# Optimization experiments

Measured on AMD Instinct MI355X. Metric: run time of the kernel, lower is better.

## Reference

```python
import jax, jax.numpy as jnp
import numpy as np

VOCAB = 32000
DIM = 1024
DFF = 4096
NLLM = 3
B, S = 2, 2048
THRESH = 0.98
EPS = 1e-8


def setup_inputs() -> dict:
    key = jax.random.key(0)
    ks = jax.random.split(key, 5)
    x = jax.random.randint(ks[0], (B, S), 0, VOCAB)
    emb = 0.02 * jax.random.normal(ks[1], (VOCAB, DIM), jnp.float32)
    ln_g = jnp.ones((NLLM, DIM), jnp.float32)
    ln_b = jnp.zeros((NLLM, DIM), jnp.float32)
    W1 = 0.002 * jax.random.normal(ks[2], (NLLM, DIM, DFF), jnp.float32)
    b1 = jnp.zeros((NLLM, DFF), jnp.float32)
    W2 = 0.002 * jax.random.normal(ks[3], (NLLM, DFF, DIM), jnp.float32)
    b2 = jnp.zeros((NLLM, DIM), jnp.float32)
    W_out = (1.0 / np.sqrt(DIM)) * jax.random.normal(ks[4], (VOCAB, DIM), jnp.float32)
    return dict(x=x, emb=emb, ln_g=ln_g, ln_b=ln_b, W1=W1, b1=b1, W2=W2, b2=b2, W_out=W_out)


def _layernorm(h, g, b):
    m = jnp.mean(h, axis=-1, keepdims=True)
    v = jnp.var(h, axis=-1, keepdims=True)
    return (h - m) * jax.lax.rsqrt(v + 1e-5) * g + b


def reference(x, emb, ln_g, ln_b, W1, b1, W2, b2, W_out):
    # Cascaded early-exit ensemble. The torch code physically re-packs surviving
    # tokens; since each LLM block here is per-token (residual MLP), a masked
    # formulation computes identical per-token math and is jit-compatible.
    Bb, Ss = x.shape
    T = Bb * Ss
    h = emb[x.reshape(T)]                      # [T, D] token embeddings
    active = jnp.ones((T,), dtype=bool)
    final = jnp.zeros((T, VOCAB), dtype=h.dtype)
    for i in range(NLLM):                      # fixed, small number of LLMs
        hn = _layernorm(h, ln_g[i], ln_b[i])
        mlp = jax.nn.gelu(hn @ W1[i] + b1[i]) @ W2[i] + b2[i]
        h_out = h + mlp                        # [T, D]
        logits = h_out @ W_out.T               # [T, V] shared output head
        cos = jnp.sum(h * h_out, axis=-1) / (
            jnp.linalg.norm(h, axis=-1) * jnp.linalg.norm(h_out, axis=-1) + EPS)
        is_last = (i == NLLM - 1)
        should_exit = cos >= THRESH
        take = active if is_last else (active & should_exit)
        final = jnp.where(take[:, None], logits, final)   # scatter logits for exiting tokens
        active = active & (~take)
        h = jnp.where(active[:, None], h_out, h)          # continuing tokens carry h_out forward
    return final.reshape(Bb, Ss, VOCAB)
```

## Files before the change

kernel.cpp:

```cpp
#include <hip/hip_runtime.h>
#include <hip/hip_bf16.h>
#include <stdint.h>

constexpr int TK   = 4096;
constexpr int DIMC = 1024;
constexpr int DFFC = 4096;
constexpr int VOC  = 32000;
constexpr int NL   = 3;

typedef __attribute__((ext_vector_type(8))) short bf16x8;
typedef __attribute__((ext_vector_type(8))) _Float16 half8;
typedef __attribute__((ext_vector_type(4))) float f32x4;
using u16 = unsigned short;

__device__ __forceinline__ u16 f2bf(float f) {
  unsigned int u = __float_as_uint(f);
  u += 0x7FFF + ((u >> 16) & 1);
  return (u16)(u >> 16);
}

__device__ __forceinline__ void split16(float v, u16& hi, u16& lo) {
  _Float16 a = (_Float16)v;
  _Float16 b = (_Float16)(v - (float)a);
  hi = __builtin_bit_cast(u16, a);
  lo = __builtin_bit_cast(u16, b);
}

__device__ __forceinline__ float gelu_f(float x) {
  float x3 = x * x * x;
  return 0.5f * x * (1.0f + tanhf(0.7978845608028654f * (x + 0.044715f * x3)));
}

__device__ __forceinline__ void gll16(const void* g, void* l) {
  __builtin_amdgcn_global_load_lds(
      (const __attribute__((address_space(1))) unsigned int*)g,
      (__attribute__((address_space(3))) unsigned int*)l, 16, 0, 0);
}

__global__ __launch_bounds__(256) void k_init(const int* __restrict__ x,
    const float* __restrict__ emb, float* __restrict__ h,
    int* __restrict__ surv, int* __restrict__ cnts) {
  const int t = blockIdx.x, tid = threadIdx.x;
  if (t == 0 && tid < 16) cnts[tid] = (tid == 12) ? TK : 0;
  if (tid == 0) surv[t] = t;
  const int tok = x[t];
  ((float4*)(h + (size_t)t * DIMC))[tid] =
      ((const float4*)(emb + (size_t)tok * DIMC))[tid];
}

__global__ __launch_bounds__(256) void k_ln(const float* __restrict__ h,
    const int* __restrict__ surv, const int* __restrict__ pM,
    const float* __restrict__ g, const float* __restrict__ b,
    u16* __restrict__ hn1, u16* __restrict__ hn2) {
  const int bidx = blockIdx.x;
  if (bidx >= *pM) return;
  const int t = surv[bidx];
  const int tid = threadIdx.x;
  const int lane = tid & 63, wid = tid >> 6;
  __shared__ float sm[4];
  float4 v = ((const float4*)(h + (size_t)t * DIMC))[tid];
  float s = v.x + v.y + v.z + v.w;
#pragma unroll
  for (int o = 32; o; o >>= 1) s += __shfl_down(s, o);
  if (lane == 0) sm[wid] = s;
  __syncthreads();
  const float mean = (sm[0] + sm[1] + sm[2] + sm[3]) * (1.0f / DIMC);
  __syncthreads();
  float4 d;
  d.x = v.x - mean; d.y = v.y - mean; d.z = v.z - mean; d.w = v.w - mean;
  float q = d.x * d.x + d.y * d.y + d.z * d.z + d.w * d.w;
#pragma unroll
  for (int o = 32; o; o >>= 1) q += __shfl_down(q, o);
  if (lane == 0) sm[wid] = q;
  __syncthreads();
  const float var = (sm[0] + sm[1] + sm[2] + sm[3]) * (1.0f / DIMC);
  const float rstd = 1.0f / sqrtf(var + 1e-5f);
  float4 gg = ((const float4*)g)[tid];
  float4 bb = ((const float4*)b)[tid];
  float o4[4];
  o4[0] = (d.x * rstd * gg.x + bb.x) * 16.f;
  o4[1] = (d.y * rstd * gg.y + bb.y) * 16.f;
  o4[2] = (d.z * rstd * gg.z + bb.z) * 16.f;
  o4[3] = (d.w * rstd * gg.w + bb.w) * 16.f;
  ushort4 u1, u2;
  split16(o4[0], u1.x, u2.x); split16(o4[1], u1.y, u2.y);
  split16(o4[2], u1.z, u2.z); split16(o4[3], u1.w, u2.w);
  ((ushort4*)(hn1 + (size_t)bidx * DIMC))[tid] = u1;
  ((ushort4*)(hn2 + (size_t)bidx * DIMC))[tid] = u2;
}

__global__ __launch_bounds__(256) void k_splitw_all(
    const float* __restrict__ W1, const float* __restrict__ W2,
    u16* __restrict__ W1all, u16* __restrict__ W2all)
{
  int bid = blockIdx.x;
  const int s = bid >> 11; bid &= 2047;
  const int tens = bid >> 10; bid &= 1023;
  const float* W; int K, N; u16 *O1, *O2; int bk, bn;
  if (tens == 0) {
    W = W1 + (size_t)s * DIMC * DFFC; K = DIMC; N = DFFC;
    O1 = W1all + (size_t)s * 2 * DFFC * DIMC;
    O2 = O1 + (size_t)DFFC * DIMC;
    bk = (bid & 15) * 64; bn = (bid >> 4) * 64;
  } else {
    W = W2 + (size_t)s * DFFC * DIMC; K = DFFC; N = DIMC;
    O1 = W2all + (size_t)s * 2 * DIMC * DFFC;
    O2 = O1 + (size_t)DIMC * DFFC;
    bk = (bid >> 4) * 64; bn = (bid & 15) * 64;
  }
  __shared__ float t[64][65];
  const int lx = threadIdx.x & 63, ly = threadIdx.x >> 6;
#pragma unroll
  for (int i = 0; i < 64; i += 4)
    t[ly + i][lx] = W[(size_t)(bk + ly + i) * N + bn + lx];
  __syncthreads();
  const int n4 = threadIdx.x >> 4;
  const int kq = (threadIdx.x & 15) * 4;
#pragma unroll
  for (int j = 0; j < 4; ++j) {
    const int n = j * 16 + n4;
    ushort4 h1, h2;
    {
      float v0 = t[kq + 0][n] * 256.f, v1 = t[kq + 1][n] * 256.f;
      float v2 = t[kq + 2][n] * 256.f, v3 = t[kq + 3][n] * 256.f;
      split16(v0, h1.x, h2.x); split16(v1, h1.y, h2.y);
      split16(v2, h1.z, h2.z); split16(v3, h1.w, h2.w);
    }
    const size_t o = (size_t)(bn + n) * K + bk + kq;
    *(ushort4*)&O1[o] = h1;
    *(ushort4*)&O2[o] = h2;
  }
}

__global__ __launch_bounds__(256) void k_cvtb(const float* __restrict__ in,
    u16* __restrict__ o, int n4) {
  int i = blockIdx.x * blockDim.x + threadIdx.x;
  const int stride = gridDim.x * blockDim.x;
  for (; i < n4; i += stride) {
    float4 v = ((const float4*)in)[i];
    ushort4 u;
    u.x = f2bf(v.x); u.y = f2bf(v.y); u.z = f2bf(v.z); u.w = f2bf(v.w);
    ((ushort4*)o)[i] = u;
  }
}

__global__ __launch_bounds__(512, 1) void k_mlp1(
    const u16* __restrict__ wsb,
    int offA, int pstrA,
    int offB, int pstrB,
    const int* __restrict__ pM,
    const float* __restrict__ bias,
    u16* __restrict__ O1, u16* __restrict__ O2)
{
  const int x = blockIdx.x & 7, g = blockIdx.x >> 3;
  const int rb = g & 15;
  const int cb = x * 2 + (g >> 4);
  const int M = *pM;
  if (rb * 256 >= M) return;
  const int n0 = cb * 256;

  __shared__ u16 S[2][32768];
  const int tid = threadIdx.x, w = tid >> 6, l = tid & 63;
  const int lr16 = l & 15, hi = l >> 4;

  int goff[8];
#pragma unroll
  for (int q = 0; q < 8; ++q) {
    const int bi = w * 8 + q;
    const int side = bi >> 5;
    const int pl = (bi >> 4) & 1;
    const int j = bi & 15;
    const int row = (side ? n0 : rb * 256) + j * 16 + lr16;
    const int base = side ? (offB + pl * pstrB) : (offA + pl * pstrA);
    goff[q] = base + row * DIMC + hi * 8;
  }

  const int wr = w >> 2, wc = w & 3;
  f32x4 acc[8][4];
#pragma unroll
  for (int mi = 0; mi < 8; ++mi)
#pragma unroll
    for (int ni = 0; ni < 4; ++ni) acc[mi][ni] = (f32x4){0.f, 0.f, 0.f, 0.f};

  auto STAGE = [&](int buf, int kt) {
#pragma unroll
    for (int q = 0; q < 8; ++q)
      gll16(wsb + (size_t)(goff[q] + kt * 32), (void*)&S[buf][(w * 8 + q) * 512]);
  };

  STAGE(0, 0);
  STAGE(1, 1);
  const int NT = DIMC / 32;
  for (int kt = 0; kt < NT; ++kt) {
    const int cur = kt & 1;
    if (kt + 1 < NT) asm volatile("s_waitcnt vmcnt(8)" ::: "memory");
    else             asm volatile("s_waitcnt vmcnt(0)" ::: "memory");
    __builtin_amdgcn_s_barrier();
    half8 b1v[4], b2v[4];
#pragma unroll
    for (int ni = 0; ni < 4; ++ni) {
      const int sub = (32 + wc * 4 + ni) * 512 + l * 8;
      b1v[ni] = *(const half8*)&S[cur][sub];
      b2v[ni] = *(const half8*)&S[cur][sub + 8192];
    }
#pragma unroll
    for (int mh = 0; mh < 2; ++mh) {
      half8 a1v[4], a2v[4];
#pragma unroll
      for (int i = 0; i < 4; ++i) {
        const int sub = (wr * 8 + mh * 4 + i) * 512 + l * 8;
        a1v[i] = *(const half8*)&S[cur][sub];
        a2v[i] = *(const half8*)&S[cur][sub + 8192];
      }
      __builtin_amdgcn_s_setprio(1);
#pragma unroll
      for (int i = 0; i < 4; ++i)
#pragma unroll
        for (int ni = 0; ni < 4; ++ni) {
          f32x4 c = acc[mh * 4 + i][ni];
          c = __builtin_amdgcn_mfma_f32_16x16x32_f16(a2v[i], b1v[ni], c, 0, 0, 0);
          c = __builtin_amdgcn_mfma_f32_16x16x32_f16(a1v[i], b2v[ni], c, 0, 0, 0);
          c = __builtin_amdgcn_mfma_f32_16x16x32_f16(a1v[i], b1v[ni], c, 0, 0, 0);
          acc[mh * 4 + i][ni] = c;
        }
      __builtin_amdgcn_s_setprio(0);
    }
    asm volatile("s_waitcnt lgkmcnt(0)" ::: "memory");
    __builtin_amdgcn_s_barrier();
    if (kt + 2 < NT) STAGE(cur, kt + 2);
  }

#pragma unroll
  for (int mi = 0; mi < 8; ++mi)
#pragma unroll
    for (int ni = 0; ni < 4; ++ni) {
      const int n = n0 + wc * 64 + ni * 16 + lr16;
#pragma unroll
      for (int r = 0; r < 4; ++r) {
        const int m = rb * 256 + wr * 128 + mi * 16 + hi * 4 + r;
        float v = gelu_f(acc[mi][ni][r] * (1.f / 4096.f) + bias[n]) * 64.f;
        u16 h1, h2; split16(v, h1, h2);
        O1[(size_t)m * DFFC + n] = h1;
        O2[(size_t)m * DFFC + n] = h2;
      }
    }
}

__global__ __launch_bounds__(512, 1) void k_mlp2(
    const u16* __restrict__ wsb,
    int offA, int pstrA,
    int offB, int pstrB,
    const int* __restrict__ pM,
    float* __restrict__ PO)
{
  const int x = blockIdx.x & 7, g = blockIdx.x >> 3;
  const int rb = g & 15;
  const int cz = x * 2 + (g >> 4);
  const int cb = cz & 7, z = cz >> 3;
  const int M = *pM;
  if (rb * 256 >= M) return;
  const int n0 = cb * 128;
  const int kz = z * 2048;

  __shared__ u16 S[3][24576];
  const int tid = threadIdx.x, w = tid >> 6, l = tid & 63;
  const int lr16 = l & 15, hi = l >> 4;

  int goff[6];
#pragma unroll
  for (int q = 0; q < 6; ++q) {
    const int bi = w * 6 + q;
    int base, row;
    if (bi < 32) {
      const int pl = bi >> 4, j = bi & 15;
      base = offA + pl * pstrA;
      row = rb * 256 + j * 16 + lr16;
    } else {
      const int bb = bi - 32, pl = bb >> 3, j = bb & 7;
      base = offB + pl * pstrB;
      row = n0 + j * 16 + lr16;
    }
    goff[q] = base + row * DFFC + kz + hi * 8;
  }

  const int wr = w >> 1, wc = w & 1;
  f32x4 acc[4][4];
#pragma unroll
  for (int mi = 0; mi < 4; ++mi)
#pragma unroll
    for (int ni = 0; ni < 4; ++ni) acc[mi][ni] = (f32x4){0.f, 0.f, 0.f, 0.f};

  auto STAGE = [&](int buf, int kt) {
#pragma unroll
    for (int q = 0; q < 6; ++q)
      gll16(wsb + (size_t)(goff[q] + kt * 32), (void*)&S[buf][(w * 6 + q) * 512]);
  };

  STAGE(0, 0);
  STAGE(1, 1);
  STAGE(2, 2);
  const int NT = 2048 / 32;
  int cur = 0;
  for (int kt = 0; kt < NT; ++kt) {
    if (kt + 2 < NT)      asm volatile("s_waitcnt vmcnt(12)" ::: "memory");
    else if (kt + 1 < NT) asm volatile("s_waitcnt vmcnt(6)" ::: "memory");
    else                  asm volatile("s_waitcnt vmcnt(0)" ::: "memory");
    __builtin_amdgcn_s_barrier();
    half8 a1v[4], a2v[4], b1v[4], b2v[4];
#pragma unroll
    for (int mi = 0; mi < 4; ++mi) {
      const int sub = (wr * 4 + mi) * 512 + l * 8;
      a1v[mi] = *(const half8*)&S[cur][sub];
      a2v[mi] = *(const half8*)&S[cur][sub + 8192];
    }
#pragma unroll
    for (int ni = 0; ni < 4; ++ni) {
      const int sub = (32 + wc * 4 + ni) * 512 + l * 8;
      b1v[ni] = *(const half8*)&S[cur][sub];
      b2v[ni] = *(const half8*)&S[cur][sub + 4096];
    }
    __builtin_amdgcn_s_setprio(1);
#pragma unroll
    for (int mi = 0; mi < 4; ++mi)
#pragma unroll
      for (int ni = 0; ni < 4; ++ni) {
        f32x4 c = acc[mi][ni];
        c = __builtin_amdgcn_mfma_f32_16x16x32_f16(a2v[mi], b1v[ni], c, 0, 0, 0);
        c = __builtin_amdgcn_mfma_f32_16x16x32_f16(a1v[mi], b2v[ni], c, 0, 0, 0);
        c = __builtin_amdgcn_mfma_f32_16x16x32_f16(a1v[mi], b1v[ni], c, 0, 0, 0);
        acc[mi][ni] = c;
      }
    __builtin_amdgcn_s_setprio(0);
    asm volatile("s_waitcnt lgkmcnt(0)" ::: "memory");
    __builtin_amdgcn_s_barrier();
    if (kt + 3 < NT) STAGE(cur, kt + 3);
    cur = (cur == 2) ? 0 : cur + 1;
  }

#pragma unroll
  for (int mi = 0; mi < 4; ++mi)
#pragma unroll
    for (int ni = 0; ni < 4; ++ni) {
      const int n = n0 + wc * 64 + ni * 16 + lr16;
#pragma unroll
      for (int r = 0; r < 4; ++r) {
        const int m = rb * 256 + wr * 64 + mi * 16 + hi * 4 + r;
        PO[(size_t)(z * TK + m) * DIMC + n] = acc[mi][ni][r] * (1.f / 16384.f);
      }
    }
}

__global__ __launch_bounds__(256) void k_decide(
    float* __restrict__ h, const float* __restrict__ p,
    const float* __restrict__ bias,
    const int* __restrict__ surv_in, int* __restrict__ surv_out,
    const int* __restrict__ pM, int* __restrict__ cnts,
    int* __restrict__ exit_idx, u16* __restrict__ hexit,
    int stage)
{
  const int bidx = blockIdx.x;
  if (bidx >= *pM) return;
  const int t = surv_in[bidx];
  const int tid = threadIdx.x;
  const int lane = tid & 63, wid = tid >> 6;
  __shared__ float sm[12];
  __shared__ int sif[2];
  float4 a  = ((const float4*)(h + (size_t)t * DIMC))[tid];
  float4 p0 = ((const float4*)(p + (size_t)bidx * DIMC))[tid];
  float4 p1 = ((const float4*)(p + (size_t)(TK + bidx) * DIMC))[tid];
  float4 bb = ((const float4*)bias)[tid];
  float4 o;
  o.x = a.x + p0.x + p1.x + bb.x;
  o.y = a.y + p0.y + p1.y + bb.y;
  o.z = a.z + p0.z + p1.z + bb.z;
  o.w = a.w + p0.w + p1.w + bb.w;
  float hh = a.x * a.x + a.y * a.y + a.z * a.z + a.w * a.w;
  float ho = a.x * o.x + a.y * o.y + a.z * o.z + a.w * o.w;
  float oo = o.x * o.x + o.y * o.y + o.z * o.z + o.w * o.w;
#pragma unroll
  for (int off = 32; off; off >>= 1) {
    hh += __shfl_down(hh, off);
    ho += __shfl_down(ho, off);
    oo += __shfl_down(oo, off);
  }
  if (lane == 0) { sm[wid] = hh; sm[4 + wid] = ho; sm[8 + wid] = oo; }
  __syncthreads();
  if (tid == 0) {
    int take;
    if (stage == NL - 1) take = 1;
    else {
      const float HH = sm[0] + sm[1] + sm[2] + sm[3];
      const float HO = sm[4] + sm[5] + sm[6] + sm[7];
      const float OO = sm[8] + sm[9] + sm[10] + sm[11];
      const float cosv = HO / (sqrtf(HH) * sqrtf(OO) + 1e-8f);
      take = (cosv >= 0.98f) ? 1 : 0;
    }
    int pos;
    if (take) {
      pos = atomicAdd(&cnts[stage], 1);
      exit_idx[pos] = t;
    } else {
      pos = atomicAdd(&cnts[4 + stage], 1);
      surv_out[pos] = t;
    }
    sif[0] = take; sif[1] = pos;
  }
  __syncthreads();
  if (sif[0]) {
    u16* dst = hexit + (size_t)sif[1] * DIMC;
    ushort4 u;
    u.x = f2bf(o.x); u.y = f2bf(o.y); u.z = f2bf(o.z); u.w = f2bf(o.w);
    ((ushort4*)dst)[tid] = u;
  } else {
    ((float4*)(h + (size_t)t * DIMC))[tid] = o;
  }
}

__global__ __launch_bounds__(512, 4) void k_logits(
    const u16* __restrict__ wsb, int offA, int offB,
    const int* __restrict__ pcnt,
    const int* __restrict__ exit_idx,
    float* __restrict__ out)
{
  const int x = blockIdx.x & 7, g = blockIdx.x >> 3;
  const int rb = g & 15;
  const int cb = x * 32 + (g >> 4);
  if (cb >= VOC / 128) return;
  const int cnt = *pcnt;
  if (rb * 256 >= cnt) return;
  const int n0 = cb * 128;

  __shared__ u16 S[3][12288];
  const int tid = threadIdx.x, w = tid >> 6, l = tid & 63;
  const int lr16 = l & 15, hi = l >> 4;

  int goff[3], loff[3];
#pragma unroll
  for (int q = 0; q < 3; ++q) {
    const int bi = w * 3 + q;
    if (bi < 16) {
      goff[q] = offA + (rb * 256 + bi * 16 + lr16) * DIMC + hi * 8;
      loff[q] = bi * 512;
    } else {
      const int j = bi - 16;
      goff[q] = offB + (n0 + j * 16 + lr16) * DIMC + hi * 8;
      loff[q] = 8192 + j * 512;
    }
  }

  const int wr = w >> 1, wc = w & 1;
  f32x4 acc[4][4];
#pragma unroll
  for (int mi = 0; mi < 4; ++mi)
#pragma unroll
    for (int ni = 0; ni < 4; ++ni) acc[mi][ni] = (f32x4){0.f, 0.f, 0.f, 0.f};

  auto STAGE = [&](int buf, int kt) {
#pragma unroll
    for (int q = 0; q < 3; ++q)
      gll16(wsb + (size_t)(goff[q] + kt * 32), (void*)&S[buf][loff[q]]);
  };

  STAGE(0, 0);
  STAGE(1, 1);
  STAGE(2, 2);
  const int NT = DIMC / 32;
  int cur = 0;
  for (int kt = 0; kt < NT; ++kt) {
    if (kt + 2 < NT)      asm volatile("s_waitcnt vmcnt(6)" ::: "memory");
    else if (kt + 1 < NT) asm volatile("s_waitcnt vmcnt(3)" ::: "memory");
    else                  asm volatile("s_waitcnt vmcnt(0)" ::: "memory");
    __builtin_amdgcn_s_barrier();
    bf16x8 aF[4], bF[4];
#pragma unroll
    for (int mi = 0; mi < 4; ++mi)
      aF[mi] = *(const bf16x8*)&S[cur][(wr * 4 + mi) * 512 + l * 8];
#pragma unroll
    for (int ni = 0; ni < 4; ++ni)
      bF[ni] = *(const bf16x8*)&S[cur][8192 + (wc * 4 + ni) * 512 + l * 8];
    __builtin_amdgcn_s_setprio(1);
#pragma unroll
    for (int mi = 0; mi < 4; ++mi)
#pragma unroll
      for (int ni = 0; ni < 4; ++ni)
        acc[mi][ni] = __builtin_amdgcn_mfma_f32_16x16x32_bf16(aF[mi], bF[ni], acc[mi][ni], 0, 0, 0);
    __builtin_amdgcn_s_setprio(0);
    asm volatile("s_waitcnt lgkmcnt(0)" ::: "memory");
    __builtin_amdgcn_s_barrier();
    if (kt + 3 < NT) STAGE(cur, kt + 3);
    cur = (cur == 2) ? 0 : cur + 1;
  }

  const int mvalid = cnt - rb * 256;
#pragma unroll
  for (int mi = 0; mi < 4; ++mi)
#pragma unroll
    for (int r = 0; r < 4; ++r) {
      const int mrow = wr * 64 + mi * 16 + hi * 4 + r;
      if (mrow < mvalid) {
        const int tok = exit_idx[rb * 256 + mrow];
        float* orow = out + (size_t)tok * VOC + n0 + wc * 64 + lr16;
#pragma unroll
        for (int ni = 0; ni < 4; ++ni)
          __builtin_nontemporal_store(acc[mi][ni][r], &orow[ni * 16]);
      }
    }
}

extern "C" void kernel_launch(void* const* d_in, const int* in_sizes, int n_in,
                              void* d_out, int out_size, void* d_ws, size_t ws_size,
                              hipStream_t stream)
{
  const int*   x    = (const int*)d_in[0];
  const float* emb  = (const float*)d_in[1];
  const float* ln_g = (const float*)d_in[2];
  const float* ln_b = (const float*)d_in[3];
  const float* W1   = (const float*)d_in[4];
  const float* b1   = (const float*)d_in[5];
  const float* W2   = (const float*)d_in[6];
  const float* b2   = (const float*)d_in[7];
  const float* Wout = (const float*)d_in[8];
  float* out = (float*)d_out;

  char* p = (char*)d_ws;
  size_t off = 0;
  auto alloc = [&](size_t bytes) -> void* {
    void* r = p + off;
    off += (bytes + 255) & ~(size_t)255;
    return r;
  };
  u16* wsb = (u16*)d_ws;
  float* h    = (float*)alloc((size_t)TK * DIMC * 4);
  float* pbuf = (float*)alloc((size_t)2 * TK * DIMC * 4);
  u16* hn1 = (u16*)pbuf;
  u16* hn2 = hn1 + (size_t)TK * DIMC;
  u16* act1 = (u16*)alloc((size_t)2 * TK * DFFC * 2);
  u16* act2 = act1 + (size_t)TK * DFFC;
  u16* Woutb = (u16*)alloc((size_t)VOC * DIMC * 2);
  u16* W1all = (u16*)alloc((size_t)NL * 2 * DFFC * DIMC * 2);
  u16* W2all = (u16*)alloc((size_t)NL * 2 * DIMC * DFFC * 2);
  u16* hexit = (u16*)alloc((size_t)TK * DIMC * 2);
  int* exit_idx = (int*)alloc((size_t)TK * 4);
  int* surv_a   = (int*)alloc((size_t)TK * 4);
  int* surv_b   = (int*)alloc((size_t)TK * 4);
  int* cnts     = (int*)alloc(64 * 4);

  const int offHn  = (int)(hn1  - wsb);
  const int offAct = (int)(act1 - wsb);
  const int offWob = (int)(Woutb- wsb);
  const int offW1a = (int)(W1all- wsb);
  const int offW2a = (int)(W2all- wsb);
  const int offHex = (int)(hexit- wsb);
  const int pstrHn  = TK * DIMC;
  const int pstrAct = TK * DFFC;
  const int pstrW   = DFFC * DIMC;

  k_init<<<TK, 256, 0, stream>>>(x, emb, h, surv_a, cnts);
  k_cvtb<<<2048, 256, 0, stream>>>(Wout, Woutb, VOC * DIMC / 4);
  k_splitw_all<<<6144, 256, 0, stream>>>(W1, W2, W1all, W2all);
  int* surv_in  = surv_a;
  int* surv_out = surv_b;
  for (int i = 0; i < NL; ++i) {
    const int* pM = (i == 0) ? (cnts + 12) : (cnts + 4 + (i - 1));
    k_ln<<<TK, 256, 0, stream>>>(h, surv_in, pM, ln_g + i * DIMC, ln_b + i * DIMC, hn1, hn2);
    k_mlp1<<<256, 512, 0, stream>>>(
        wsb, offHn, pstrHn, offW1a + i * 2 * pstrW, pstrW,
        pM, b1 + (size_t)i * DFFC, act1, act2);
    k_mlp2<<<256, 512, 0, stream>>>(
        wsb, offAct, pstrAct, offW2a + i * 2 * pstrW, pstrW, pM, pbuf);
    k_decide<<<TK, 256, 0, stream>>>(h, pbuf, b2 + (size_t)i * DIMC,
        surv_in, surv_out, pM, cnts, exit_idx, hexit, i);
    k_logits<<<4096, 512, 0, stream>>>(wsb, offHex, offWob, cnts + i, exit_idx, out);
    int* tmp = surv_in; surv_in = surv_out; surv_out = tmp;
  }
}
```

Before: 1.399 ms.

## Fuse layernorm into init/decide kernels, merge weight prep, double-buffer GEMMs

Drops the standalone layernorm kernel. The first layernorm is computed inside the embedding init kernel, and each later one is computed inside the decide kernel for continuing tokens, written at their compacted position. This saves one launch and one re-read of h per stage. The Wout bf16 conversion is merged into the weight-split kernel, and the mlp2 and logits pipelines go from triple to double buffering, which cuts LDS use but shortens prefetch depth. hn1/hn2 get their own buffer instead of aliasing pbuf, since decide now reads pbuf while writing hn.

```diff
diff --git a/kernel.cpp b/kernel.cpp
--- a/kernel.cpp
+++ b/kernel.cpp
@@ -38,27 +38,18 @@
 }
 
 __global__ __launch_bounds__(256) void k_init(const int* __restrict__ x,
-    const float* __restrict__ emb, float* __restrict__ h,
+    const float* __restrict__ emb,
+    const float* __restrict__ g, const float* __restrict__ b,
+    float* __restrict__ h, u16* __restrict__ hn1, u16* __restrict__ hn2,
     int* __restrict__ surv, int* __restrict__ cnts) {
   const int t = blockIdx.x, tid = threadIdx.x;
   if (t == 0 && tid < 16) cnts[tid] = (tid == 12) ? TK : 0;
   if (tid == 0) surv[t] = t;
   const int tok = x[t];
-  ((float4*)(h + (size_t)t * DIMC))[tid] =
-      ((const float4*)(emb + (size_t)tok * DIMC))[tid];
-}
-
-__global__ __launch_bounds__(256) void k_ln(const float* __restrict__ h,
-    const int* __restrict__ surv, const int* __restrict__ pM,
-    const float* __restrict__ g, const float* __restrict__ b,
-    u16* __restrict__ hn1, u16* __restrict__ hn2) {
-  const int bidx = blockIdx.x;
-  if (bidx >= *pM) return;
-  const int t = surv[bidx];
-  const int tid = threadIdx.x;
   const int lane = tid & 63, wid = tid >> 6;
   __shared__ float sm[4];
-  float4 v = ((const float4*)(h + (size_t)t * DIMC))[tid];
+  float4 v = ((const float4*)(emb + (size_t)tok * DIMC))[tid];
+  ((float4*)(h + (size_t)t * DIMC))[tid] = v;
   float s = v.x + v.y + v.z + v.w;
 #pragma unroll
   for (int o = 32; o; o >>= 1) s += __shfl_down(s, o);
@@ -85,15 +76,28 @@
   ushort4 u1, u2;
   split16(o4[0], u1.x, u2.x); split16(o4[1], u1.y, u2.y);
   split16(o4[2], u1.z, u2.z); split16(o4[3], u1.w, u2.w);
-  ((ushort4*)(hn1 + (size_t)bidx * DIMC))[tid] = u1;
-  ((ushort4*)(hn2 + (size_t)bidx * DIMC))[tid] = u2;
-}
-
-__global__ __launch_bounds__(256) void k_splitw_all(
+  ((ushort4*)(hn1 + (size_t)t * DIMC))[tid] = u1;
+  ((ushort4*)(hn2 + (size_t)t * DIMC))[tid] = u2;
+}
+
+__global__ __launch_bounds__(256) void k_prep(
     const float* __restrict__ W1, const float* __restrict__ W2,
-    u16* __restrict__ W1all, u16* __restrict__ W2all)
+    u16* __restrict__ W1all, u16* __restrict__ W2all,
+    const float* __restrict__ Wout, u16* __restrict__ Woutb)
 {
   int bid = blockIdx.x;
+  if (bid >= 6144) {
+    int i = (bid - 6144) * 256 + threadIdx.x;
+    const int n4 = VOC * DIMC / 4;
+    const int stride = 2048 * 256;
+    for (; i < n4; i += stride) {
+      float4 v = ((const float4*)Wout)[i];
+      ushort4 u;
+      u.x = f2bf(v.x); u.y = f2bf(v.y); u.z = f2bf(v.z); u.w = f2bf(v.w);
+      ((ushort4*)Woutb)[i] = u;
+    }
+    return;
+  }
   const int s = bid >> 11; bid &= 2047;
   const int tens = bid >> 10; bid &= 1023;
   const float* W; int K, N; u16 *O1, *O2; int bk, bn;
@@ -129,18 +133,6 @@
     const size_t o = (size_t)(bn + n) * K + bk + kq;
     *(ushort4*)&O1[o] = h1;
     *(ushort4*)&O2[o] = h2;
-  }
-}
-
-__global__ __launch_bounds__(256) void k_cvtb(const float* __restrict__ in,
-    u16* __restrict__ o, int n4) {
-  int i = blockIdx.x * blockDim.x + threadIdx.x;
-  const int stride = gridDim.x * blockDim.x;
-  for (; i < n4; i += stride) {
-    float4 v = ((const float4*)in)[i];
-    ushort4 u;
-    u.x = f2bf(v.x); u.y = f2bf(v.y); u.z = f2bf(v.z); u.w = f2bf(v.w);
-    ((ushort4*)o)[i] = u;
   }
 }
 
@@ -262,7 +254,7 @@
   const int n0 = cb * 128;
   const int kz = z * 2048;
 
-  __shared__ u16 S[3][24576];
+  __shared__ u16 S[2][24576];
   const int tid = threadIdx.x, w = tid >> 6, l = tid & 63;
   const int lr16 = l & 15, hi = l >> 4;
 
@@ -298,13 +290,11 @@
 
   STAGE(0, 0);
   STAGE(1, 1);
-  STAGE(2, 2);
   const int NT = 2048 / 32;
-  int cur = 0;
   for (int kt = 0; kt < NT; ++kt) {
-    if (kt + 2 < NT)      asm volatile("s_waitcnt vmcnt(12)" ::: "memory");
-    else if (kt + 1 < NT) asm volatile("s_waitcnt vmcnt(6)" ::: "memory");
-    else                  asm volatile("s_waitcnt vmcnt(0)" ::: "memory");
+    const int cur = kt & 1;
+    if (kt + 1 < NT) asm volatile("s_waitcnt vmcnt(6)" ::: "memory");
+    else             asm volatile("s_waitcnt vmcnt(0)" ::: "memory");
     __builtin_amdgcn_s_barrier();
     half8 a1v[4], a2v[4], b1v[4], b2v[4];
 #pragma unroll
@@ -333,8 +323,7 @@
     __builtin_amdgcn_s_setprio(0);
     asm volatile("s_waitcnt lgkmcnt(0)" ::: "memory");
     __builtin_amdgcn_s_barrier();
-    if (kt + 3 < NT) STAGE(cur, kt + 3);
-    cur = (cur == 2) ? 0 : cur + 1;
+    if (kt + 2 < NT) STAGE(cur, kt + 2);
   }
 
 #pragma unroll
@@ -356,6 +345,8 @@
     const int* __restrict__ surv_in, int* __restrict__ surv_out,
     const int* __restrict__ pM, int* __restrict__ cnts,
     int* __restrict__ exit_idx, u16* __restrict__ hexit,
+    const float* __restrict__ gnx, const float* __restrict__ bnx,
+    u16* __restrict__ hn1, u16* __restrict__ hn2,
     int stage)
 {
   const int bidx = blockIdx.x;
@@ -363,7 +354,7 @@
   const int t = surv_in[bidx];
   const int tid = threadIdx.x;
   const int lane = tid & 63, wid = tid >> 6;
-  __shared__ float sm[12];
+  __shared__ float sm[16];
   __shared__ int sif[2];
   float4 a  = ((const float4*)(h + (size_t)t * DIMC))[tid];
   float4 p0 = ((const float4*)(p + (size_t)bidx * DIMC))[tid];
@@ -377,14 +368,17 @@
   float hh = a.x * a.x + a.y * a.y + a.z * a.z + a.w * a.w;
   float ho = a.x * o.x + a.y * o.y + a.z * o.z + a.w * o.w;
   float oo = o.x * o.x + o.y * o.y + o.z * o.z + o.w * o.w;
+  float so = o.x + o.y + o.z + o.w;
 #pragma unroll
   for (int off = 32; off; off >>= 1) {
     hh += __shfl_down(hh, off);
     ho += __shfl_down(ho, off);
     oo += __shfl_down(oo, off);
-  }
-  if (lane == 0) { sm[wid] = hh; sm[4 + wid] = ho; sm[8 + wid] = oo; }
+    so += __shfl_down(so, off);
+  }
+  if (lane == 0) { sm[wid] = hh; sm[4 + wid] = ho; sm[8 + wid] = oo; sm[12 + wid] = so; }
   __syncthreads();
+  const float mean = (sm[12] + sm[13] + sm[14] + sm[15]) * (1.0f / DIMC);
   if (tid == 0) {
     int take;
     if (stage == NL - 1) take = 1;
@@ -413,6 +407,28 @@
     ((ushort4*)dst)[tid] = u;
   } else {
     ((float4*)(h + (size_t)t * DIMC))[tid] = o;
+    float4 d;
+    d.x = o.x - mean; d.y = o.y - mean; d.z = o.z - mean; d.w = o.w - mean;
+    float q = d.x * d.x + d.y * d.y + d.z * d.z + d.w * d.w;
+#pragma unroll
+    for (int off = 32; off; off >>= 1) q += __shfl_down(q, off);
+    if (lane == 0) sm[wid] = q;
+    __syncthreads();
+    const float var = (sm[0] + sm[1] + sm[2] + sm[3]) * (1.0f / DIMC);
+    const float rstd = 1.0f / sqrtf(var + 1e-5f);
+    float4 gg = ((const float4*)gnx)[tid];
+    float4 b2 = ((const float4*)bnx)[tid];
+    float o4[4];
+    o4[0] = (d.x * rstd * gg.x + b2.x) * 16.f;
+    o4[1] = (d.y * rstd * gg.y + b2.y) * 16.f;
+    o4[2] = (d.z * rstd * gg.z + b2.z) * 16.f;
+    o4[3] = (d.w * rstd * gg.w + b2.w) * 16.f;
+    ushort4 u1, u2;
+    split16(o4[0], u1.x, u2.x); split16(o4[1], u1.y, u2.y);
+    split16(o4[2], u1.z, u2.z); split16(o4[3], u1.w, u2.w);
+    const int pos = sif[1];
+    ((ushort4*)(hn1 + (size_t)pos * DIMC))[tid] = u1;
+    ((ushort4*)(hn2 + (size_t)pos * DIMC))[tid] = u2;
   }
 }
 
@@ -430,7 +446,7 @@
   if (rb * 256 >= cnt) return;
   const int n0 = cb * 128;
 
-  __shared__ u16 S[3][12288];
+  __shared__ u16 S[2][12288];
   const int tid = threadIdx.x, w = tid >> 6, l = tid & 63;
   const int lr16 = l & 15, hi = l >> 4;
 
@@ -463,13 +479,11 @@
 
   STAGE(0, 0);
   STAGE(1, 1);
-  STAGE(2, 2);
   const int NT = DIMC / 32;
-  int cur = 0;
   for (int kt = 0; kt < NT; ++kt) {
-    if (kt + 2 < NT)      asm volatile("s_waitcnt vmcnt(6)" ::: "memory");
-    else if (kt + 1 < NT) asm volatile("s_waitcnt vmcnt(3)" ::: "memory");
-    else                  asm volatile("s_waitcnt vmcnt(0)" ::: "memory");
+    const int cur = kt & 1;
+    if (kt + 1 < NT) asm volatile("s_waitcnt vmcnt(3)" ::: "memory");
+    else             asm volatile("s_waitcnt vmcnt(0)" ::: "memory");
     __builtin_amdgcn_s_barrier();
     bf16x8 aF[4], bF[4];
 #pragma unroll
@@ -487,8 +501,7 @@
     __builtin_amdgcn_s_setprio(0);
     asm volatile("s_waitcnt lgkmcnt(0)" ::: "memory");
     __builtin_amdgcn_s_barrier();
-    if (kt + 3 < NT) STAGE(cur, kt + 3);
-    cur = (cur == 2) ? 0 : cur + 1;
+    if (kt + 2 < NT) STAGE(cur, kt + 2);
   }
 
   const int mvalid = cnt - rb * 256;
@@ -532,7 +545,7 @@
   u16* wsb = (u16*)d_ws;
   float* h    = (float*)alloc((size_t)TK * DIMC * 4);
   float* pbuf = (float*)alloc((size_t)2 * TK * DIMC * 4);
-  u16* hn1 = (u16*)pbuf;
+  u16* hn1 = (u16*)alloc((size_t)2 * TK * DIMC * 2);
   u16* hn2 = hn1 + (size_t)TK * DIMC;
   u16* act1 = (u16*)alloc((size_t)2 * TK * DFFC * 2);
   u16* act2 = act1 + (size_t)TK * DFFC;
@@ -555,21 +568,21 @@
   const int pstrAct = TK * DFFC;
   const int pstrW   = DFFC * DIMC;
 
-  k_init<<<TK, 256, 0, stream>>>(x, emb, h, surv_a, cnts);
-  k_cvtb<<<2048, 256, 0, stream>>>(Wout, Woutb, VOC * DIMC / 4);
-  k_splitw_all<<<6144, 256, 0, stream>>>(W1, W2, W1all, W2all);
+  k_init<<<TK, 256, 0, stream>>>(x, emb, ln_g, ln_b, h, hn1, hn2, surv_a, cnts);
+  k_prep<<<8192, 256, 0, stream>>>(W1, W2, W1all, W2all, Wout, Woutb);
   int* surv_in  = surv_a;
   int* surv_out = surv_b;
   for (int i = 0; i < NL; ++i) {
     const int* pM = (i == 0) ? (cnts + 12) : (cnts + 4 + (i - 1));
-    k_ln<<<TK, 256, 0, stream>>>(h, surv_in, pM, ln_g + i * DIMC, ln_b + i * DIMC, hn1, hn2);
     k_mlp1<<<256, 512, 0, stream>>>(
         wsb, offHn, pstrHn, offW1a + i * 2 * pstrW, pstrW,
         pM, b1 + (size_t)i * DFFC, act1, act2);
     k_mlp2<<<256, 512, 0, stream>>>(
         wsb, offAct, pstrAct, offW2a + i * 2 * pstrW, pstrW, pM, pbuf);
+    const int inx = (i + 1 < NL) ? (i + 1) : i;
     k_decide<<<TK, 256, 0, stream>>>(h, pbuf, b2 + (size_t)i * DIMC,
-        surv_in, surv_out, pM, cnts, exit_idx, hexit, i);
+        surv_in, surv_out, pM, cnts, exit_idx, hexit,
+        ln_g + (size_t)inx * DIMC, ln_b + (size_t)inx * DIMC, hn1, hn2, i);
     k_logits<<<4096, 512, 0, stream>>>(wsb, offHex, offWob, cnts + i, exit_idx, out);
     int* tmp = surv_in; surv_in = surv_out; surv_out = tmp;
   }
```

New measurement: 1.368 ms. 2.2% less time.
